# Kernel optimization log

Hardware: AMD Instinct MI355X
Metric: run time of the kernel (lower is better)

## Reference

```python
import jax, jax.numpy as jnp
import numpy as np

E = 1024
H = 16
F = 4096
EPS = 1e-5


def layer_norm(x, gamma, beta):
    mu = jnp.mean(x, axis=-1, keepdims=True)
    var = jnp.var(x, axis=-1, keepdims=True)
    return (x - mu) * jax.lax.rsqrt(var + EPS) * gamma + beta


def setup_inputs() -> dict:
    key = jax.random.key(0)
    ks = jax.random.split(key, 12)
    s = lambda d: 1.0 / np.sqrt(d)
    x = jax.random.normal(ks[0], (2, 2048, E), dtype=jnp.float32)
    Wq = jax.random.uniform(ks[1], (E, E), minval=-s(E), maxval=s(E))
    bq = jnp.zeros((E,), jnp.float32)
    Wk = jax.random.uniform(ks[2], (E, E), minval=-s(E), maxval=s(E))
    bk = jnp.zeros((E,), jnp.float32)
    Wv = jax.random.uniform(ks[3], (E, E), minval=-s(E), maxval=s(E))
    bv = jnp.zeros((E,), jnp.float32)
    Wo = jax.random.uniform(ks[4], (E, E), minval=-s(E), maxval=s(E))
    bo = jnp.zeros((E,), jnp.float32)
    g1 = jnp.ones((E,), jnp.float32)
    b1 = jnp.zeros((E,), jnp.float32)
    W1 = jax.random.uniform(ks[5], (E, F), minval=-s(E), maxval=s(E))
    bf1 = jnp.zeros((F,), jnp.float32)
    W2 = jax.random.uniform(ks[6], (F, E), minval=-s(F), maxval=s(F))
    bf2 = jnp.zeros((E,), jnp.float32)
    g2 = jnp.ones((E,), jnp.float32)
    b2 = jnp.zeros((E,), jnp.float32)
    return dict(x=x, Wq=Wq, bq=bq, Wk=Wk, bk=bk, Wv=Wv, bv=bv, Wo=Wo, bo=bo,
                g1=g1, b1=b1, W1=W1, bf1=bf1, W2=W2, bf2=bf2, g2=g2, b2=b2)


def reference(x, Wq, bq, Wk, bk, Wv, bv, Wo, bo, g1, b1, W1, bf1, W2, bf2, g2, b2):
    B, L, _ = x.shape
    Dh = E // H
    q = (x @ Wq + bq).reshape(B, L, H, Dh).transpose(0, 2, 1, 3)  # b h l d
    k = (x @ Wk + bk).reshape(B, L, H, Dh).transpose(0, 2, 1, 3)  # computed but unused (faithful to source)
    v = (x @ Wv + bv).reshape(B, L, H, Dh).transpose(0, 2, 1, 3)
    # NOTE: source computes scores as Q @ V^T (not K), scaled, then softmax
    scores = jnp.einsum('bhqd,bhkd->bhqk', q, v) / jnp.sqrt(jnp.float32(Dh))
    att = jax.nn.softmax(scores, axis=-1)
    ctx = jnp.einsum('bhqk,bhkd->bhqd', att, v)
    ctx = ctx.transpose(0, 2, 1, 3).reshape(B, L, E)
    att_out = ctx @ Wo + bo
    post_att = layer_norm(x + att_out, g1, b1)
    ff = jax.nn.relu(post_att @ W1 + bf1) @ W2 + bf2
    return layer_norm(post_att + ff, g2, b2)
```

## Files before the change

kernel.cpp:

```cpp
#include <hip/hip_runtime.h>
#include <stdint.h>

typedef unsigned short u16;
typedef __attribute__((ext_vector_type(8))) short short8;
typedef __attribute__((ext_vector_type(4))) float f32x4;
typedef __attribute__((ext_vector_type(4))) unsigned short u16x4;

#define TOKENS 4096
#define E_DIM 1024
#define F_DIM 4096
#define SEQ 2048
#define NH 16
#define DH 64

__device__ __forceinline__ u16 f2b(float f) {
  union { float f; unsigned u; } v; v.f = f;
  unsigned r = v.u + 0x7fffu + ((v.u >> 16) & 1u);
  return (u16)(r >> 16);
}

__device__ __forceinline__ void gl2lds16(const u16* g, u16* l) {
  __builtin_amdgcn_global_load_lds(
      (const __attribute__((address_space(1))) unsigned int*)(size_t)(g),
      (__attribute__((address_space(3))) unsigned int*)(unsigned int)(size_t)(l),
      16, 0, 0);
}

__global__ __launch_bounds__(256)
void transpose_w(const float* __restrict__ W, u16* __restrict__ Wt, int K, int N) {
  __shared__ float tile[32][33];
  const int kb = blockIdx.x * 32, nb = blockIdx.y * 32;
  const int tx = threadIdx.x & 31, ty = threadIdx.x >> 5;
#pragma unroll
  for (int i = 0; i < 32; i += 8)
    tile[ty + i][tx] = W[(size_t)(kb + ty + i) * N + nb + tx];
  __syncthreads();
#pragma unroll
  for (int i = 0; i < 32; i += 8)
    Wt[(size_t)(nb + ty + i) * K + kb + tx] = f2b(tile[tx][ty + i]);
}

__global__ __launch_bounds__(256)
void f32_to_bf16(const float* __restrict__ in, u16* __restrict__ out) {
  const int i = blockIdx.x * 256 + threadIdx.x;
  f32x4 f = ((const f32x4*)in)[i];
  u16x4 u;
#pragma unroll
  for (int j = 0; j < 4; j++) u[j] = f2b(f[j]);
  ((u16x4*)out)[i] = u;
}

__global__ __launch_bounds__(256)
void transpose_v(const u16* __restrict__ vsrc, u16* __restrict__ vt) {
  __shared__ u16 tile[64][66];
  const int kb = blockIdx.x * 64;
  const int bh = blockIdx.y;
  const int b = bh >> 4, h = bh & 15;
  {
    const int d = threadIdx.x & 63, r = threadIdx.x >> 6;
#pragma unroll
    for (int i = 0; i < 64; i += 4)
      tile[r + i][d] = vsrc[(size_t)(b * SEQ + kb + r + i) * E_DIM + h * DH + d];
  }
  __syncthreads();
  {
    const int pos = threadIdx.x & 63;
    const int srck = (pos & 3) * 16 + (pos >> 2);
#pragma unroll
    for (int j = 0; j < 64; j += 4) {
      const int d = (threadIdx.x >> 6) + j;
      vt[(size_t)(bh * DH + d) * SEQ + kb + pos] = tile[srck][d];
    }
  }
}

template <int RELU, int OUTBF>
__global__ __launch_bounds__(256)
void gemm_bt(const u16* __restrict__ A, const u16* __restrict__ Bt,
             const float* __restrict__ bias, void* __restrict__ Cout,
             int M, int N, int K) {
  __shared__ __align__(16) u16 As[128 * 32];
  __shared__ __align__(16) u16 Bs[128 * 32];
  const int tid = threadIdx.x;
  const int lane = tid & 63, wave = tid >> 6;
  const int mBlk = blockIdx.y * 128, nBlk = blockIdx.x * 128;
  const int wm = (wave >> 1) * 64, wn = (wave & 1) * 64;
  const int l15 = lane & 15, g = lane >> 4;

  f32x4 acc[4][4] = {};
  const int srow = lane >> 2;
  const int scol = (lane & 3) * 8;

  const u16* Ab = A + (size_t)mBlk * K;
  const u16* Bb = Bt + (size_t)nBlk * K;

  for (int k0 = 0; k0 < K; k0 += 32) {
    __syncthreads();
    for (int c = wave; c < 8; c += 4) {
      const int r = c * 16 + srow;
      gl2lds16(Ab + (size_t)r * K + k0 + scol, As + c * 512 + lane * 8);
      gl2lds16(Bb + (size_t)r * K + k0 + scol, Bs + c * 512 + lane * 8);
    }
    __syncthreads();

    short8 af[4], bf[4];
#pragma unroll
    for (int i = 0; i < 4; i++)
      af[i] = *(const short8*)(As + (wm + i * 16 + l15) * 32 + g * 8);
#pragma unroll
    for (int i = 0; i < 4; i++)
      bf[i] = *(const short8*)(Bs + (wn + i * 16 + l15) * 32 + g * 8);
#pragma unroll
    for (int mi = 0; mi < 4; mi++)
#pragma unroll
      for (int ni = 0; ni < 4; ni++)
        acc[mi][ni] = __builtin_amdgcn_mfma_f32_16x16x32_bf16(af[mi], bf[ni],
                                                              acc[mi][ni], 0, 0, 0);
  }

  const int row0 = mBlk + wm + g * 4;
  const int col0 = nBlk + wn + l15;
#pragma unroll
  for (int ni = 0; ni < 4; ni++) {
    const int c = col0 + ni * 16;
    const float bv = bias[c];
#pragma unroll
    for (int mi = 0; mi < 4; mi++) {
#pragma unroll
      for (int r = 0; r < 4; r++) {
        float v = acc[mi][ni][r] + bv;
        if (RELU) v = fmaxf(v, 0.f);
        const size_t idx = (size_t)(row0 + mi * 16 + r) * N + c;
        if (OUTBF) ((u16*)Cout)[idx] = f2b(v);
        else       ((float*)Cout)[idx] = v;
      }
    }
  }
}

__global__ __launch_bounds__(256)
void gemm_bt_sk(const u16* __restrict__ A, const u16* __restrict__ Bt,
                const float* __restrict__ bias, float* __restrict__ Cout,
                int M, int N, int K) {
  __shared__ __align__(16) u16 As[128 * 32];
  __shared__ __align__(16) u16 Bs[128 * 32];
  const int tid = threadIdx.x;
  const int lane = tid & 63, wave = tid >> 6;
  const int mBlk = blockIdx.y * 128, nBlk = blockIdx.x * 128;
  const int kz = blockIdx.z;
  const int Kh = K >> 1;
  const int wm = (wave >> 1) * 64, wn = (wave & 1) * 64;
  const int l15 = lane & 15, g = lane >> 4;

  f32x4 acc[4][4] = {};
  const int srow = lane >> 2;
  const int scol = (lane & 3) * 8;

  const u16* Ab = A + (size_t)mBlk * K + (size_t)kz * Kh;
  const u16* Bb = Bt + (size_t)nBlk * K + (size_t)kz * Kh;

  for (int k0 = 0; k0 < Kh; k0 += 32) {
    __syncthreads();
    for (int c = wave; c < 8; c += 4) {
      const int r = c * 16 + srow;
      gl2lds16(Ab + (size_t)r * K + k0 + scol, As + c * 512 + lane * 8);
      gl2lds16(Bb + (size_t)r * K + k0 + scol, Bs + c * 512 + lane * 8);
    }
    __syncthreads();

    short8 af[4], bf[4];
#pragma unroll
    for (int i = 0; i < 4; i++)
      af[i] = *(const short8*)(As + (wm + i * 16 + l15) * 32 + g * 8);
#pragma unroll
    for (int i = 0; i < 4; i++)
      bf[i] = *(const short8*)(Bs + (wn + i * 16 + l15) * 32 + g * 8);
#pragma unroll
    for (int mi = 0; mi < 4; mi++)
#pragma unroll
      for (int ni = 0; ni < 4; ni++)
        acc[mi][ni] = __builtin_amdgcn_mfma_f32_16x16x32_bf16(af[mi], bf[ni],
                                                              acc[mi][ni], 0, 0, 0);
  }

  float* out = Cout + (size_t)kz * M * N;
  const int row0 = mBlk + wm + g * 4;
  const int col0 = nBlk + wn + l15;
#pragma unroll
  for (int ni = 0; ni < 4; ni++) {
    const int c = col0 + ni * 16;
    const float bv = (kz == 0) ? bias[c] : 0.f;
#pragma unroll
    for (int mi = 0; mi < 4; mi++) {
#pragma unroll
      for (int r = 0; r < 4; r++)
        out[(size_t)(row0 + mi * 16 + r) * N + c] = acc[mi][ni][r] + bv;
    }
  }
}

__global__ __launch_bounds__(256)
void gemm_qv64(const u16* __restrict__ A, const u16* __restrict__ Bqv,
               const float* __restrict__ bq, const float* __restrict__ bv,
               u16* __restrict__ qout, u16* __restrict__ vout, int K) {
  __shared__ __align__(16) u16 As[128 * 32];
  __shared__ __align__(16) u16 Bs[64 * 32];
  const int tid = threadIdx.x;
  const int lane = tid & 63, wave = tid >> 6;
  const int mBlk = blockIdx.y * 128, nBlk = blockIdx.x * 64;
  const int isQ = nBlk < 1024;
  const int ncol = isQ ? nBlk : nBlk - 1024;
  const float* bias = isQ ? bq : bv;
  u16* out = isQ ? qout : vout;
  const float oscale = isQ ? 0.125f : 1.0f;
  const int wm = (wave >> 1) * 64, wn = (wave & 1) * 32;
  const int l15 = lane & 15, g = lane >> 4;

  f32x4 acc[4][2] = {};
  const int srow = lane >> 2;
  const int scol = (lane & 3) * 8;

  const u16* Ab = A + (size_t)mBlk * K;
  const u16* Bb = Bqv + (size_t)nBlk * K;

  for (int k0 = 0; k0 < K; k0 += 32) {
    __syncthreads();
    for (int c = wave; c < 8; c += 4) {
      const int r = c * 16 + srow;
      gl2lds16(Ab + (size_t)r * K + k0 + scol, As + c * 512 + lane * 8);
    }
    gl2lds16(Bb + (size_t)(wave * 16 + srow) * K + k0 + scol, Bs + wave * 512 + lane * 8);
    __syncthreads();

    short8 af[4], bf[2];
#pragma unroll
    for (int i = 0; i < 4; i++)
      af[i] = *(const short8*)(As + (wm + i * 16 + l15) * 32 + g * 8);
#pragma unroll
    for (int i = 0; i < 2; i++)
      bf[i] = *(const short8*)(Bs + (wn + i * 16 + l15) * 32 + g * 8);
#pragma unroll
    for (int mi = 0; mi < 4; mi++)
#pragma unroll
      for (int ni = 0; ni < 2; ni++)
        acc[mi][ni] = __builtin_amdgcn_mfma_f32_16x16x32_bf16(af[mi], bf[ni],
                                                              acc[mi][ni], 0, 0, 0);
  }

  const int row0 = mBlk + wm + g * 4;
  const int col0 = ncol + wn + l15;
#pragma unroll
  for (int ni = 0; ni < 2; ni++) {
    const int c = col0 + ni * 16;
    const float bv_ = bias[c];
#pragma unroll
    for (int mi = 0; mi < 4; mi++) {
#pragma unroll
      for (int r = 0; r < 4; r++) {
        float v = (acc[mi][ni][r] + bv_) * oscale;
        out[(size_t)(row0 + mi * 16 + r) * E_DIM + c] = f2b(v);
      }
    }
  }
}

__global__ __launch_bounds__(128)
void attn_kernel(const u16* __restrict__ qb, const u16* __restrict__ vb,
                 const u16* __restrict__ vtb, u16* __restrict__ ctxb) {
  __shared__ __align__(16) u16 Vs[2][64 * 64];
  __shared__ __align__(16) u16 Vts[2][64 * 64];
  __shared__ __align__(16) u16 Pl[2][32 * 64];
  const int tid = threadIdx.x;
  const int lane = tid & 63;
  const int wave = tid >> 6;
  const int l15 = lane & 15;
  const int g = lane >> 4;
  const int qblk = blockIdx.x;
  const int bh = blockIdx.y;
  const int b = bh >> 4;
  const int h = bh & 15;
  const int qrow = qblk * 64 + wave * 32;

  short8 aq[2][2];
#pragma unroll
  for (int sub = 0; sub < 2; sub++) {
    const u16* qp = qb + ((size_t)(b * SEQ + qrow + sub * 16 + l15)) * E_DIM + h * DH + g * 8;
    aq[sub][0] = *(const short8*)(qp);
    aq[sub][1] = *(const short8*)(qp + 32);
  }

  f32x4 o[2][4] = {};
  float lsum[2][4] = {};

  const u16* vbase = vb + ((size_t)b * SEQ) * E_DIM + h * DH;
  const u16* vtbase = vtb + ((size_t)bh * DH) * SEQ;
  u16* myPl = Pl[wave];

  const int srow = tid >> 3;
  const int sch = tid & 7;

#define STAGE(buf, kcv)                                                          \
  {                                                                              \
    const int kc_ = (kcv);                                                       \
    _Pragma("unroll") for (int j = 0; j < 4; j++) {                              \
      const int key = j * 16 + srow;                                             \
      gl2lds16(vbase + (size_t)(kc_ + key) * E_DIM + ((sch ^ (key & 7)) * 8),    \
               Vs[buf] + key * 64 + sch * 8);                                    \
      const int d = j * 16 + srow;                                               \
      gl2lds16(vtbase + (size_t)d * SEQ + kc_ + ((sch ^ (d & 7)) * 8),           \
               Vts[buf] + d * 64 + sch * 8);                                     \
    }                                                                            \
  }

  STAGE(0, 0)
  int cur = 0;

  for (int kc = 0; kc < SEQ; kc += 64) {
    asm volatile("s_barrier" ::: "memory");
    if (kc + 64 < SEQ) {
      STAGE(cur ^ 1, kc + 64)
      asm volatile("s_waitcnt vmcnt(8)" ::: "memory");
    } else {
      asm volatile("s_waitcnt vmcnt(0)" ::: "memory");
    }
    asm volatile("s_barrier" ::: "memory");

    const u16* VsC = Vs[cur];
    const u16* VtsC = Vts[cur];

    f32x4 s[2][4];
#pragma unroll
    for (int nt = 0; nt < 4; nt++) {
      const int key = nt * 16 + l15;
      const u16* vr = VsC + key * 64;
      short8 b0 = *(const short8*)(vr + ((g ^ (key & 7)) * 8));
      short8 b1 = *(const short8*)(vr + (((4 + g) ^ (key & 7)) * 8));
      f32x4 z0 = {}, z1 = {};
      z0 = __builtin_amdgcn_mfma_f32_16x16x32_bf16(aq[0][0], b0, z0, 0, 0, 0);
      z0 = __builtin_amdgcn_mfma_f32_16x16x32_bf16(aq[0][1], b1, z0, 0, 0, 0);
      z1 = __builtin_amdgcn_mfma_f32_16x16x32_bf16(aq[1][0], b0, z1, 0, 0, 0);
      z1 = __builtin_amdgcn_mfma_f32_16x16x32_bf16(aq[1][1], b1, z1, 0, 0, 0);
      s[0][nt] = z0;
      s[1][nt] = z1;
    }

#pragma unroll
    for (int sub = 0; sub < 2; sub++) {
#pragma unroll
      for (int r = 0; r < 4; r++) {
        const int row = sub * 16 + g * 4 + r;
        union { float f; unsigned u; } p0, p1, p2, p3;
        p0.f = __expf(s[sub][0][r]);
        p1.f = __expf(s[sub][1][r]);
        p2.f = __expf(s[sub][2][r]);
        p3.f = __expf(s[sub][3][r]);
        union { unsigned u; float f; } t0, t1, t2, t3;
        t0.u = p0.u & 0xffff0000u;
        t1.u = p1.u & 0xffff0000u;
        t2.u = p2.u & 0xffff0000u;
        t3.u = p3.u & 0xffff0000u;
        lsum[sub][r] += (t0.f + t1.f) + (t2.f + t3.f);
        uint2 pk;
        pk.x = __builtin_amdgcn_perm(p1.u, p0.u, 0x07060302u);
        pk.y = __builtin_amdgcn_perm(p3.u, p2.u, 0x07060302u);
        *(uint2*)(myPl + row * 64 + (((l15 >> 1) ^ (row & 7)) << 3) + ((l15 & 1) << 2)) = pk;
      }
    }

#pragma unroll
    for (int ks = 0; ks < 2; ks++) {
      const int row0_ = l15, row1_ = 16 + l15;
      short8 ap0 = *(const short8*)(myPl + row0_ * 64 + (((ks * 4 + g) ^ (row0_ & 7)) << 3));
      short8 ap1 = *(const short8*)(myPl + row1_ * 64 + (((ks * 4 + g) ^ (row1_ & 7)) << 3));
#pragma unroll
      for (int dt = 0; dt < 4; dt++) {
        const int d = dt * 16 + l15;
        short8 bv = *(const short8*)(VtsC + d * 64 + (((ks * 4 + g) ^ (d & 7)) * 8));
        o[0][dt] = __builtin_amdgcn_mfma_f32_16x16x32_bf16(ap0, bv, o[0][dt], 0, 0, 0);
        o[1][dt] = __builtin_amdgcn_mfma_f32_16x16x32_bf16(ap1, bv, o[1][dt], 0, 0, 0);
      }
    }
    cur ^= 1;
  }
#undef STAGE

#pragma unroll
  for (int sub = 0; sub < 2; sub++) {
#pragma unroll
    for (int r = 0; r < 4; r++) {
      float l = lsum[sub][r];
      l += __shfl_xor(l, 1);
      l += __shfl_xor(l, 2);
      l += __shfl_xor(l, 4);
      l += __shfl_xor(l, 8);
      const float inv = 1.0f / l;
      size_t base = ((size_t)(b * SEQ + qrow + sub * 16 + g * 4 + r)) * E_DIM + h * DH;
#pragma unroll
      for (int dt = 0; dt < 4; dt++)
        ctxb[base + dt * 16 + l15] = f2b(o[sub][dt][r] * inv);
    }
  }
}

__global__ __launch_bounds__(256)
void add_ln3(const float* __restrict__ X, const float* __restrict__ Y0,
             const float* __restrict__ Y1,
             const float* __restrict__ gam, const float* __restrict__ bet,
             float* __restrict__ out32, u16* __restrict__ out16) {
  const int row = blockIdx.x;
  const int tid = threadIdx.x;
  const size_t base = (size_t)row * E_DIM;
  float v[4];
  float s = 0.f, sq = 0.f;
#pragma unroll
  for (int i = 0; i < 4; i++) {
    const int c = tid + i * 256;
    float x = X[base + c] + Y0[base + c] + Y1[base + c];
    v[i] = x; s += x; sq += x * x;
  }
#pragma unroll
  for (int off = 32; off; off >>= 1) {
    s += __shfl_xor(s, off);
    sq += __shfl_xor(sq, off);
  }
  __shared__ float sh[8];
  const int wave = tid >> 6, lane = tid & 63;
  if (lane == 0) { sh[wave] = s; sh[4 + wave] = sq; }
  __syncthreads();
  s = sh[0] + sh[1] + sh[2] + sh[3];
  sq = sh[4] + sh[5] + sh[6] + sh[7];
  const float mean = s * (1.f / 1024.f);
  const float var = sq * (1.f / 1024.f) - mean * mean;
  const float rstd = rsqrtf(var + 1e-5f);
#pragma unroll
  for (int i = 0; i < 4; i++) {
    const int c = tid + i * 256;
    float y = (v[i] - mean) * rstd * gam[c] + bet[c];
    out32[base + c] = y;
    if (out16) out16[base + c] = f2b(y);
  }
}

extern "C" void kernel_launch(void* const* d_in, const int* in_sizes, int n_in,
                              void* d_out, int out_size, void* d_ws, size_t ws_size,
                              hipStream_t stream) {
  const float* x   = (const float*)d_in[0];
  const float* Wq  = (const float*)d_in[1];
  const float* bq  = (const float*)d_in[2];
  const float* Wv  = (const float*)d_in[5];
  const float* bv  = (const float*)d_in[6];
  const float* Wo  = (const float*)d_in[7];
  const float* bo  = (const float*)d_in[8];
  const float* g1  = (const float*)d_in[9];
  const float* b1  = (const float*)d_in[10];
  const float* W1  = (const float*)d_in[11];
  const float* bf1 = (const float*)d_in[12];
  const float* W2  = (const float*)d_in[13];
  const float* bf2 = (const float*)d_in[14];
  const float* g2  = (const float*)d_in[15];
  const float* b2  = (const float*)d_in[16];

  char* w = (char*)d_ws;
  const size_t MB = 1024ull * 1024ull;
  u16*   xb   = (u16*)(w + 0);
  u16*   h1   = (u16*)(w + 8 * MB);
  u16*   qb   = (u16*)(w + 8 * MB);
  u16*   vb   = (u16*)(w + 16 * MB);
  u16*   vtb  = (u16*)(w + 24 * MB);
  u16*   ctxb = (u16*)(w + 32 * MB);
  float* att0 = (float*)(w + 40 * MB);
  float* ff0  = (float*)(w + 40 * MB);
  float* pa   = (float*)(w + 72 * MB);
  u16*   pab  = (u16*)(w + 88 * MB);
  u16*   WqT  = (u16*)(w + 96 * MB);
  u16*   WvT  = (u16*)(w + 98 * MB);
  u16*   WoT  = (u16*)(w + 100 * MB);
  u16*   W1T  = (u16*)(w + 102 * MB);
  u16*   W2T  = (u16*)(w + 110 * MB);

  transpose_w<<<dim3(32, 32), 256, 0, stream>>>(Wq, WqT, 1024, 1024);
  transpose_w<<<dim3(32, 32), 256, 0, stream>>>(Wv, WvT, 1024, 1024);
  transpose_w<<<dim3(32, 32), 256, 0, stream>>>(Wo, WoT, 1024, 1024);
  transpose_w<<<dim3(32, 128), 256, 0, stream>>>(W1, W1T, 1024, 4096);
  transpose_w<<<dim3(128, 32), 256, 0, stream>>>(W2, W2T, 4096, 1024);
  f32_to_bf16<<<TOKENS * E_DIM / 4 / 256, 256, 0, stream>>>(x, xb);

  gemm_qv64<<<dim3(32, 32), 256, 0, stream>>>(xb, WqT, bq, bv, qb, vb, 1024);
  transpose_v<<<dim3(32, 32), 256, 0, stream>>>(vb, vtb);
  attn_kernel<<<dim3(32, 32), 128, 0, stream>>>(qb, vb, vtb, ctxb);
  gemm_bt_sk<<<dim3(8, 32, 2), 256, 0, stream>>>(ctxb, WoT, bo, att0, TOKENS, 1024, 1024);
  add_ln3<<<TOKENS, 256, 0, stream>>>(x, att0, att0 + (size_t)TOKENS * 1024, g1, b1, pa, pab);
  gemm_bt<1, 1><<<dim3(32, 32), 256, 0, stream>>>(pab, W1T, bf1, h1, TOKENS, 4096, 1024);
  gemm_bt_sk<<<dim3(8, 32, 2), 256, 0, stream>>>(h1, W2T, bf2, ff0, TOKENS, 1024, 4096);
  add_ln3<<<TOKENS, 256, 0, stream>>>(pa, ff0, ff0 + (size_t)TOKENS * 1024, g2, b2, (float*)d_out, (u16*)nullptr);
}
```

Before: 382.4 us.

## Replace FFN1 GEMM with 256x256-tile, triple-buffered, XCD-swizzled 512-thread kernel

Adds a new GEMM kernel with 256x256 output tiles, 8 waves per block, and a three-stage LDS ring filled by direct global-to-LDS loads. A and B staging is interleaved with the two MFMA half-steps and uses setprio around the MFMA bursts. Block IDs are remapped so neighbouring tiles land on the same XCD for L2 reuse, and the kernel is used for the W1 projection (4096x4096x1024). The larger tile cuts global and LDS traffic per FLOP, at the cost of 128 accumulator registers per thread, lower occupancy, and only 256 blocks for 256 CUs.

```diff
diff --git a/kernel.cpp b/kernel.cpp
--- a/kernel.cpp
+++ b/kernel.cpp
@@ -133,6 +133,125 @@
         const size_t idx = (size_t)(row0 + mi * 16 + r) * N + c;
         if (OUTBF) ((u16*)Cout)[idx] = f2b(v);
         else       ((float*)Cout)[idx] = v;
+      }
+    }
+  }
+}
+
+template <int RELU, int OUTBF>
+__global__ __launch_bounds__(512)
+void gemm256(const u16* __restrict__ A, const u16* __restrict__ Bt,
+             const float* __restrict__ bias, void* __restrict__ Cout,
+             int N, int K) {
+  __shared__ __align__(16) u16 lds[3][2][8192];
+  const int tid = threadIdx.x;
+  const int lane = tid & 63, wave = tid >> 6;
+  const int wm = wave >> 2, wn = wave & 3;
+  const int l15 = lane & 15, g = lane >> 4;
+
+  const int bid = blockIdx.x;
+  const int xcd = bid & 7, idx = bid >> 3;
+  const int mT = (xcd >> 2) * 8 + (idx >> 2);
+  const int nT = (xcd & 3) * 4 + (idx & 3);
+  const int mBlk = mT * 256, nBlk = nT * 256;
+
+  const u16* Ab = A + (size_t)mBlk * K;
+  const u16* Bb = Bt + (size_t)nBlk * K;
+
+  const int sm = lane >> 2;
+  const int sk = (lane & 3) * 8;
+  const u16* sa0 = Ab + (size_t)(wave * 16 + sm) * K + sk;
+  const u16* sa1 = Ab + (size_t)((8 + wave) * 16 + sm) * K + sk;
+  const u16* sb0 = Bb + (size_t)(wave * 16 + sm) * K + sk;
+  const u16* sb1 = Bb + (size_t)((8 + wave) * 16 + sm) * K + sk;
+
+  f32x4 acc[8][4] = {};
+
+  const int NT = K >> 5;
+
+#define STAGE_A(buf, t)                                             \
+  {                                                                 \
+    gl2lds16(sa0 + (size_t)(t) * 32, &lds[buf][0][wave * 512 + lane * 8]);       \
+    gl2lds16(sa1 + (size_t)(t) * 32, &lds[buf][0][(8 + wave) * 512 + lane * 8]); \
+  }
+#define STAGE_B(buf, t)                                             \
+  {                                                                 \
+    gl2lds16(sb0 + (size_t)(t) * 32, &lds[buf][1][wave * 512 + lane * 8]);       \
+    gl2lds16(sb1 + (size_t)(t) * 32, &lds[buf][1][(8 + wave) * 512 + lane * 8]); \
+  }
+
+  STAGE_A(0, 0) STAGE_B(0, 0)
+  STAGE_A(1, 1) STAGE_B(1, 1)
+  asm volatile("s_waitcnt vmcnt(4)" ::: "memory");
+  asm volatile("s_barrier" ::: "memory");
+
+  int buf = 0, sbuf = 2;
+  for (int t = 0; t < NT; ++t) {
+    const u16* As_ = &lds[buf][0][wm * (8 * 512)];
+    const u16* Bs_ = &lds[buf][1][wn * (4 * 512)];
+    const int fo = l15 * 32 + g * 8;
+
+    short8 af[4], bfr[4];
+#pragma unroll
+    for (int i = 0; i < 4; i++)
+      af[i] = *(const short8*)(As_ + i * 512 + fo);
+#pragma unroll
+    for (int i = 0; i < 4; i++)
+      bfr[i] = *(const short8*)(Bs_ + i * 512 + fo);
+    if (t + 2 < NT) STAGE_A(sbuf, t + 2)
+    asm volatile("s_barrier" ::: "memory");
+    asm volatile("s_waitcnt lgkmcnt(0)" ::: "memory");
+    __builtin_amdgcn_sched_barrier(0);
+    __builtin_amdgcn_s_setprio(1);
+#pragma unroll
+    for (int mg = 0; mg < 4; mg++)
+#pragma unroll
+      for (int ng = 0; ng < 4; ng++)
+        acc[mg][ng] = __builtin_amdgcn_mfma_f32_16x16x32_bf16(af[mg], bfr[ng],
+                                                              acc[mg][ng], 0, 0, 0);
+    __builtin_amdgcn_s_setprio(0);
+    asm volatile("s_barrier" ::: "memory");
+
+#pragma unroll
+    for (int i = 0; i < 4; i++)
+      af[i] = *(const short8*)(As_ + (4 + i) * 512 + fo);
+    if (t + 2 < NT) STAGE_B(sbuf, t + 2)
+    asm volatile("s_barrier" ::: "memory");
+    asm volatile("s_waitcnt lgkmcnt(0)" ::: "memory");
+    __builtin_amdgcn_sched_barrier(0);
+    __builtin_amdgcn_s_setprio(1);
+#pragma unroll
+    for (int mg = 0; mg < 4; mg++)
+#pragma unroll
+      for (int ng = 0; ng < 4; ng++)
+        acc[4 + mg][ng] = __builtin_amdgcn_mfma_f32_16x16x32_bf16(af[mg], bfr[ng],
+                                                                  acc[4 + mg][ng], 0, 0, 0);
+    __builtin_amdgcn_s_setprio(0);
+    if (t + 2 < NT) asm volatile("s_waitcnt vmcnt(4)" ::: "memory");
+    else            asm volatile("s_waitcnt vmcnt(0)" ::: "memory");
+    asm volatile("s_barrier" ::: "memory");
+
+    buf = (buf == 2) ? 0 : buf + 1;
+    sbuf = (sbuf == 2) ? 0 : sbuf + 1;
+  }
+#undef STAGE_A
+#undef STAGE_B
+
+  const int row0 = mBlk + wm * 128 + g * 4;
+  const int col0 = nBlk + wn * 64 + l15;
+#pragma unroll
+  for (int ng = 0; ng < 4; ng++) {
+    const int c = col0 + ng * 16;
+    const float bv = bias[c];
+#pragma unroll
+    for (int mg = 0; mg < 8; mg++) {
+#pragma unroll
+      for (int r = 0; r < 4; r++) {
+        float v = acc[mg][ng][r] + bv;
+        if (RELU) v = fmaxf(v, 0.f);
+        const size_t o = (size_t)(row0 + mg * 16 + r) * N + c;
+        if (OUTBF) ((u16*)Cout)[o] = f2b(v);
+        else       ((float*)Cout)[o] = v;
       }
     }
   }
@@ -490,7 +609,7 @@
   attn_kernel<<<dim3(32, 32), 128, 0, stream>>>(qb, vb, vtb, ctxb);
   gemm_bt_sk<<<dim3(8, 32, 2), 256, 0, stream>>>(ctxb, WoT, bo, att0, TOKENS, 1024, 1024);
   add_ln3<<<TOKENS, 256, 0, stream>>>(x, att0, att0 + (size_t)TOKENS * 1024, g1, b1, pa, pab);
-  gemm_bt<1, 1><<<dim3(32, 32), 256, 0, stream>>>(pab, W1T, bf1, h1, TOKENS, 4096, 1024);
+  gemm256<1, 1><<<dim3(256), 512, 0, stream>>>(pab, W1T, bf1, h1, 4096, 1024);
   gemm_bt_sk<<<dim3(8, 32, 2), 256, 0, stream>>>(h1, W2T, bf2, ff0, TOKENS, 1024, 4096);
   add_ln3<<<TOKENS, 256, 0, stream>>>(pa, ff0, ff0 + (size_t)TOKENS * 1024, g2, b2, (float*)d_out, (u16*)nullptr);
 }
```

New measurement: 381.2 us. About the same (-0.3%).
